# Optimization experiments

Measured on AMD Instinct MI355X. Metric: run time of the kernel, lower is better.

## Reference

```python
import jax, jax.numpy as jnp
import numpy as np

C = 32
C_Z = 128
S = 256   # MSA depth
N = 384   # residues


def setup_inputs() -> dict:
    key = jax.random.key(0)
    ks = jax.random.split(key, 7)
    m = jax.random.normal(ks[0], (S, N, C), dtype=jnp.float32)
    gamma = jnp.ones((C,), dtype=jnp.float32)
    beta = jnp.zeros((C,), dtype=jnp.float32)
    # projections stored as [in, out]
    W1 = jax.random.normal(ks[1], (C, C), dtype=jnp.float32) / np.sqrt(C)
    W2 = jax.random.normal(ks[2], (C, C), dtype=jnp.float32) / np.sqrt(C)
    W3 = jax.random.normal(ks[3], (C * C, C_Z), dtype=jnp.float32) / np.sqrt(C * C)
    b3 = jnp.zeros((C_Z,), dtype=jnp.float32)
    return {"m": m, "gamma": gamma, "beta": beta, "W1": W1, "W2": W2, "W3": W3, "b3": b3}


def reference(m, gamma, beta, W1, W2, W3, b3):
    # LayerNorm over channel dim
    mu = jnp.mean(m, axis=-1, keepdims=True)
    var = jnp.mean(jnp.square(m - mu), axis=-1, keepdims=True)
    mn = (m - mu) * jax.lax.rsqrt(var + 1e-5) * gamma + beta
    a = jnp.einsum('sic,cd->sid', mn, W1)  # [s, n, c]
    b = jnp.einsum('sic,cd->sid', mn, W2)  # [s, n, c]
    # outer product, mean over MSA dim s -> [n, n, c, c]
    o = jnp.einsum('sic,sjd->ijcd', a, b) / a.shape[0]
    o = o.reshape(o.shape[0], o.shape[1], C * C)  # [n, n, c*c]
    z = o @ W3 + b3  # [n, n, c_z]
    return z
```

## Files before the change

kernel.cpp:

```cpp
#include <hip/hip_runtime.h>

#define S_DEPTH 256
#define NRES 384
#define CIN 32
#define CZ 128
#define MDIM (NRES * CIN)

typedef short bf16x8 __attribute__((ext_vector_type(8)));
typedef short short4v __attribute__((ext_vector_type(4)));
typedef float f32x4 __attribute__((ext_vector_type(4)));

static __device__ __forceinline__ unsigned short f2bf(float f) {
  unsigned int u = __float_as_uint(f);
  unsigned int r = (u + 0x7fffu + ((u >> 16) & 1u)) >> 16;
  return (unsigned short)r;
}

static __device__ __forceinline__ void gld16(const void* g, void* l) {
  __builtin_amdgcn_global_load_lds((__attribute__((address_space(1))) void*)(g),
                                   (__attribute__((address_space(3))) void*)(l),
                                   16, 0, 0);
}

__global__ __launch_bounds__(256) void k_pre(
    const float* __restrict__ mm, const float* __restrict__ gamma,
    const float* __restrict__ beta, const float* __restrict__ W1,
    const float* __restrict__ W2, const float* __restrict__ W3,
    unsigned short* __restrict__ aT, unsigned short* __restrict__ bT,
    unsigned short* __restrict__ W3T) {
  __shared__ __align__(16) char sraw[256 * 33 * 4];
  const int t = threadIdx.x;

  if (blockIdx.x < 16) {
    unsigned short (*tile)[72] = (unsigned short(*)[72])sraw;
    const int b = blockIdx.x;
    const int d0 = (b & 7) * 4;
    const int e0 = (b >> 3) * 64;
#pragma unroll
    for (int iter = 0; iter < 32; ++iter) {
      int lr_ = iter * 4 + (t >> 6);
      int c = lr_ >> 2, dl = lr_ & 3;
      int q = c * 32 + d0 + dl;
      tile[lr_][t & 63] = f2bf(W3[q * 128 + e0 + (t & 63)]);
    }
    __syncthreads();
    const int e_l = t >> 2;
    const int dl = t & 3;
    unsigned short* dst = W3T + (((size_t)(d0 + dl) * 128) + e0 + e_l) * 32;
#pragma unroll
    for (int j = 0; j < 32; ++j) dst[j] = tile[j * 4 + dl][e_l];
    return;
  }

  float* buf = (float*)sraw;
  const int i = blockIdx.x - 16;

#pragma unroll
  for (int it = 0; it < 8; ++it) {
    int s = it * 32 + (t >> 3);
    int c4 = (t & 7) * 4;
    const float4 v = *(const float4*)(mm + ((size_t)s * NRES + i) * CIN + c4);
    buf[s * 33 + c4 + 0] = v.x;
    buf[s * 33 + c4 + 1] = v.y;
    buf[s * 33 + c4 + 2] = v.z;
    buf[s * 33 + c4 + 3] = v.w;
  }
  __syncthreads();

  float x[32];
#pragma unroll
  for (int k = 0; k < 32; ++k) x[k] = buf[t * 33 + k];
  float mu = 0.f;
#pragma unroll
  for (int k = 0; k < 32; ++k) mu += x[k];
  mu *= (1.f / 32.f);
  float var = 0.f;
#pragma unroll
  for (int k = 0; k < 32; ++k) {
    float dk = x[k] - mu;
    var += dk * dk;
  }
  var *= (1.f / 32.f);
  float inv = rsqrtf(var + 1e-5f);
#pragma unroll
  for (int k = 0; k < 32; ++k) x[k] = (x[k] - mu) * inv * gamma[k] + beta[k];

  float va[32], vb[32];
#pragma unroll
  for (int c = 0; c < 32; ++c) { va[c] = 0.f; vb[c] = 0.f; }
#pragma unroll
  for (int k = 0; k < 32; ++k) {
    float xk = x[k];
#pragma unroll
    for (int c = 0; c < 32; ++c) va[c] += xk * W1[k * 32 + c];
#pragma unroll
    for (int c = 0; c < 32; ++c) vb[c] += xk * W2[k * 32 + c];
  }

  unsigned short* dstA = aT + ((size_t)(t >> 6) * MDIM + (size_t)i * 32) * 64 + (t & 63);
  unsigned short* dstB = bT + ((size_t)(t >> 6) * MDIM + (size_t)i * 32) * 64 + (t & 63);
#pragma unroll
  for (int c = 0; c < 32; ++c) dstA[c * 64] = f2bf(va[c]);
#pragma unroll
  for (int c = 0; c < 32; ++c) dstB[c * 64] = f2bf(vb[c]);
}

__global__ __launch_bounds__(512, 2) void k_opm(
    const unsigned short* __restrict__ aT, const unsigned short* __restrict__ bT,
    const unsigned short* __restrict__ W3T, const float* __restrict__ b3,
    float* __restrict__ out) {
  __shared__ __align__(16) char smem[131072];
  const int t = threadIdx.x;
  const int w = t >> 6;
  const int l = t & 63;
  const int lr = l & 15;
  const int quad = l >> 4;
  const int wm = w >> 2, wn = w & 3;

  const int g = blockIdx.x;
  const int xcd = g & 7;
  const int rr = g >> 3;
  const int bx = rr / 6;
  const int by = xcd * 6 + (rr - bx * 6);
  const int m0 = by * 256;
  const int n0 = bx * 256;

  f32x4 acc[8][4];
#pragma unroll
  for (int mt = 0; mt < 8; ++mt)
#pragma unroll
    for (int nt = 0; nt < 4; ++nt) {
      acc[mt][nt][0] = 0.f; acc[mt][nt][1] = 0.f;
      acc[mt][nt][2] = 0.f; acc[mt][nt][3] = 0.f;
    }

  char* smemB = smem + 32768;
  const int laneoff = (l >> 3) * 64 + (((l & 7) ^ (l >> 3)) * 8);
  const int r8 = lr & 7;

  for (int k0 = 0; k0 < 256; k0 += 64) {
    __syncthreads();
    const unsigned short* aSlab = aT + ((size_t)(k0 >> 6) * MDIM + m0) * 64;
    const unsigned short* bSlab = bT + ((size_t)(k0 >> 6) * MDIM + n0) * 64;
#pragma unroll
    for (int p_ = 0; p_ < 4; ++p_) {
      int ch = p_ * 8 + w;
      gld16(aSlab + ch * 512 + laneoff, smem + ch * 1024);
    }
#pragma unroll
    for (int p_ = 0; p_ < 4; ++p_) {
      int ch = p_ * 8 + w;
      gld16(bSlab + ch * 512 + laneoff, smemB + ch * 1024);
    }
    __syncthreads();

#pragma unroll
    for (int ks = 0; ks < 2; ++ks) {
      const int segoff = (((ks * 4 + quad) ^ r8) << 4);
      bf16x8 af[8];
#pragma unroll
      for (int mt = 0; mt < 8; ++mt) {
        int chunk = wm * 16 + mt * 2 + (lr >> 3);
        af[mt] = *(const bf16x8*)(smem + chunk * 1024 + r8 * 128 + segoff);
      }
#pragma unroll
      for (int nt = 0; nt < 4; ++nt) {
        int chunk = wn * 8 + nt * 2 + (lr >> 3);
        bf16x8 bfr = *(const bf16x8*)(smemB + chunk * 1024 + r8 * 128 + segoff);
#pragma unroll
        for (int mt = 0; mt < 8; ++mt)
          acc[mt][nt] =
              __builtin_amdgcn_mfma_f32_16x16x32_bf16(af[mt], bfr, acc[mt][nt], 0, 0, 0);
      }
    }
  }

  __syncthreads();
  const float scale = 1.0f / 256.0f;
#pragma unroll
  for (int mt = 0; mt < 8; ++mt) {
    int i_l = wm * 4 + (mt >> 1);
    int chc = 2 * (mt & 1) + (quad >> 1);
#pragma unroll
    for (int nt = 0; nt < 4; ++nt) {
      int j_l = wn * 2 + (nt >> 1);
      int d = (nt & 1) * 16 + lr;
      int p = i_l * 8 + j_l;
      int ch = d * 4 + chc;
      int key = (p ^ d) & 7;
      int off = p * 2048 + ((ch ^ key) << 4) + 8 * (quad & 1);
      short4v pk;
      pk[0] = (short)f2bf(acc[mt][nt][0] * scale);
      pk[1] = (short)f2bf(acc[mt][nt][1] * scale);
      pk[2] = (short)f2bf(acc[mt][nt][2] * scale);
      pk[3] = (short)f2bf(acc[mt][nt][3] * scale);
      *(short4v*)(smem + off) = pk;
    }
  }
  __syncthreads();

  f32x4 zacc[4];
#pragma unroll
  for (int a = 0; a < 4; ++a) {
    zacc[a][0] = 0.f; zacc[a][1] = 0.f; zacc[a][2] = 0.f; zacc[a][3] = 0.f;
  }
  const float bias = b3[w * 16 + lr];

  const unsigned short* wg = W3T + (size_t)(w * 16 + lr) * 32 + quad * 8;

  bf16x8 wcur = *(const bf16x8*)(wg);
#pragma unroll
  for (int kq = 0; kq < 32; ++kq) {
    bf16x8 wnxt;
    if (kq < 31) wnxt = *(const bf16x8*)(wg + (size_t)(kq + 1) * 4096);
    bf16x8 aef[4];
#pragma unroll
    for (int mte = 0; mte < 4; ++mte) {
      int row = mte * 16 + lr;
      int ch = kq * 4 + quad;
      int key = (row ^ kq) & 7;
      aef[mte] = *(const bf16x8*)(smem + row * 2048 + ((ch ^ key) << 4));
    }
#pragma unroll
    for (int mte = 0; mte < 4; ++mte)
      zacc[mte] = __builtin_amdgcn_mfma_f32_16x16x32_bf16(aef[mte], wcur, zacc[mte], 0, 0, 0);
    wcur = wnxt;
  }

  const int i0 = by * 8, j0 = bx * 8;
  const int e = w * 16 + lr;
#pragma unroll
  for (int mte = 0; mte < 4; ++mte)
#pragma unroll
    for (int r = 0; r < 4; ++r) {
      int p = mte * 16 + quad * 4 + r;
      out[(((size_t)(i0 + (p >> 3))) * NRES + (j0 + (p & 7))) * CZ + e] =
          zacc[mte][r] + bias;
    }
}

extern "C" void kernel_launch(void* const* d_in, const int* in_sizes, int n_in,
                              void* d_out, int out_size, void* d_ws, size_t ws_size,
                              hipStream_t stream) {
  const float* m = (const float*)d_in[0];
  const float* gamma = (const float*)d_in[1];
  const float* beta = (const float*)d_in[2];
  const float* W1 = (const float*)d_in[3];
  const float* W2 = (const float*)d_in[4];
  const float* W3 = (const float*)d_in[5];
  const float* b3 = (const float*)d_in[6];
  float* out = (float*)d_out;

  unsigned short* aT = (unsigned short*)d_ws;
  unsigned short* bT = aT + (size_t)MDIM * S_DEPTH;
  unsigned short* W3T = bT + (size_t)MDIM * S_DEPTH;

  k_pre<<<400, 256, 0, stream>>>(m, gamma, beta, W1, W2, W3, aT, bT, W3T);
  k_opm<<<2304, 512, 0, stream>>>(aT, bT, W3T, b3, out);
}
```

Measured before the change: 237.9 us.

## Double-buffer OPM K-loop, split preprocessing blocks, retile W3 projection

The main outer-product GEMM loop now double-buffers the A/B slabs in LDS, so the next K-slab loads while MFMAs run on the current one, with one barrier per iteration. The preprocessing kernel is split 4x per residue, one block per MSA-depth quarter with each thread handling 8 output channels, raising its block count to improve parallelism. The W3 projection stage is retiled so each wave computes a 2x2 MFMA tile instead of 4x1, reusing each LDS A fragment across two W3 columns. The cost is that LDS use in the GEMM phase doubles to the full 128KB, and the preprocessing now recomputes LayerNorm per channel group.

```diff
diff --git a/kernel.cpp b/kernel.cpp
--- a/kernel.cpp
+++ b/kernel.cpp
@@ -28,7 +28,7 @@
     const float* __restrict__ W2, const float* __restrict__ W3,
     unsigned short* __restrict__ aT, unsigned short* __restrict__ bT,
     unsigned short* __restrict__ W3T) {
-  __shared__ __align__(16) char sraw[256 * 33 * 4];
+  __shared__ __align__(16) char sraw[128 * 72 * 2];
   const int t = threadIdx.x;
 
   if (blockIdx.x < 16) {
@@ -53,23 +53,27 @@
   }
 
   float* buf = (float*)sraw;
-  const int i = blockIdx.x - 16;
-
-#pragma unroll
-  for (int it = 0; it < 8; ++it) {
-    int s = it * 32 + (t >> 3);
-    int c4 = (t & 7) * 4;
-    const float4 v = *(const float4*)(mm + ((size_t)s * NRES + i) * CIN + c4);
-    buf[s * 33 + c4 + 0] = v.x;
-    buf[s * 33 + c4 + 1] = v.y;
-    buf[s * 33 + c4 + 2] = v.z;
-    buf[s * 33 + c4 + 3] = v.w;
+  const int b = blockIdx.x - 16;
+  const int i = b >> 2;
+  const int g = b & 3;
+
+  {
+    int r = t >> 2, c8 = (t & 3) * 8;
+    const float* src = mm + ((size_t)(g * 64 + r) * NRES + i) * CIN + c8;
+    const float4 v0 = *(const float4*)(src);
+    const float4 v1 = *(const float4*)(src + 4);
+    float* d = buf + r * 33 + c8;
+    d[0] = v0.x; d[1] = v0.y; d[2] = v0.z; d[3] = v0.w;
+    d[4] = v1.x; d[5] = v1.y; d[6] = v1.z; d[7] = v1.w;
   }
   __syncthreads();
 
+  const int row = t & 63;
+  const int cg = t >> 6;
+
   float x[32];
 #pragma unroll
-  for (int k = 0; k < 32; ++k) x[k] = buf[t * 33 + k];
+  for (int k = 0; k < 32; ++k) x[k] = buf[row * 33 + k];
   float mu = 0.f;
 #pragma unroll
   for (int k = 0; k < 32; ++k) mu += x[k];
@@ -85,24 +89,28 @@
 #pragma unroll
   for (int k = 0; k < 32; ++k) x[k] = (x[k] - mu) * inv * gamma[k] + beta[k];
 
-  float va[32], vb[32];
-#pragma unroll
-  for (int c = 0; c < 32; ++c) { va[c] = 0.f; vb[c] = 0.f; }
+  float va[8], vb[8];
+#pragma unroll
+  for (int c = 0; c < 8; ++c) { va[c] = 0.f; vb[c] = 0.f; }
 #pragma unroll
   for (int k = 0; k < 32; ++k) {
     float xk = x[k];
-#pragma unroll
-    for (int c = 0; c < 32; ++c) va[c] += xk * W1[k * 32 + c];
-#pragma unroll
-    for (int c = 0; c < 32; ++c) vb[c] += xk * W2[k * 32 + c];
-  }
-
-  unsigned short* dstA = aT + ((size_t)(t >> 6) * MDIM + (size_t)i * 32) * 64 + (t & 63);
-  unsigned short* dstB = bT + ((size_t)(t >> 6) * MDIM + (size_t)i * 32) * 64 + (t & 63);
-#pragma unroll
-  for (int c = 0; c < 32; ++c) dstA[c * 64] = f2bf(va[c]);
-#pragma unroll
-  for (int c = 0; c < 32; ++c) dstB[c * 64] = f2bf(vb[c]);
+    const float* w1r = W1 + k * 32 + cg * 8;
+    const float* w2r = W2 + k * 32 + cg * 8;
+#pragma unroll
+    for (int c = 0; c < 8; ++c) va[c] += xk * w1r[c];
+#pragma unroll
+    for (int c = 0; c < 8; ++c) vb[c] += xk * w2r[c];
+  }
+
+  unsigned short* dstA =
+      aT + ((size_t)g * MDIM + (size_t)i * 32 + cg * 8) * 64 + row;
+  unsigned short* dstB =
+      bT + ((size_t)g * MDIM + (size_t)i * 32 + cg * 8) * 64 + row;
+#pragma unroll
+  for (int c = 0; c < 8; ++c) dstA[c * 64] = f2bf(va[c]);
+#pragma unroll
+  for (int c = 0; c < 8; ++c) dstB[c * 64] = f2bf(vb[c]);
 }
 
 __global__ __launch_bounds__(512, 2) void k_opm(
@@ -134,25 +142,35 @@
       acc[mt][nt][2] = 0.f; acc[mt][nt][3] = 0.f;
     }
 
-  char* smemB = smem + 32768;
   const int laneoff = (l >> 3) * 64 + (((l & 7) ^ (l >> 3)) * 8);
   const int r8 = lr & 7;
 
-  for (int k0 = 0; k0 < 256; k0 += 64) {
-    __syncthreads();
-    const unsigned short* aSlab = aT + ((size_t)(k0 >> 6) * MDIM + m0) * 64;
-    const unsigned short* bSlab = bT + ((size_t)(k0 >> 6) * MDIM + n0) * 64;
+  {
+    const unsigned short* aS = aT + (size_t)m0 * 64;
+    const unsigned short* bS = bT + (size_t)n0 * 64;
 #pragma unroll
     for (int p_ = 0; p_ < 4; ++p_) {
       int ch = p_ * 8 + w;
-      gld16(aSlab + ch * 512 + laneoff, smem + ch * 1024);
-    }
-#pragma unroll
-    for (int p_ = 0; p_ < 4; ++p_) {
-      int ch = p_ * 8 + w;
-      gld16(bSlab + ch * 512 + laneoff, smemB + ch * 1024);
-    }
-    __syncthreads();
+      gld16(aS + ch * 512 + laneoff, smem + ch * 1024);
+      gld16(bS + ch * 512 + laneoff, smem + 32768 + ch * 1024);
+    }
+  }
+  __syncthreads();
+
+  for (int kt = 0; kt < 4; ++kt) {
+    if (kt < 3) {
+      char* nb = smem + ((kt + 1) & 1) * 65536;
+      const unsigned short* aS = aT + ((size_t)(kt + 1) * MDIM + m0) * 64;
+      const unsigned short* bS = bT + ((size_t)(kt + 1) * MDIM + n0) * 64;
+#pragma unroll
+      for (int p_ = 0; p_ < 4; ++p_) {
+        int ch = p_ * 8 + w;
+        gld16(aS + ch * 512 + laneoff, nb + ch * 1024);
+        gld16(bS + ch * 512 + laneoff, nb + 32768 + ch * 1024);
+      }
+    }
+    const char* cb = smem + (kt & 1) * 65536;
+    const char* cbB = cb + 32768;
 
 #pragma unroll
     for (int ks = 0; ks < 2; ++ks) {
@@ -161,21 +179,21 @@
 #pragma unroll
       for (int mt = 0; mt < 8; ++mt) {
         int chunk = wm * 16 + mt * 2 + (lr >> 3);
-        af[mt] = *(const bf16x8*)(smem + chunk * 1024 + r8 * 128 + segoff);
+        af[mt] = *(const bf16x8*)(cb + chunk * 1024 + r8 * 128 + segoff);
       }
 #pragma unroll
       for (int nt = 0; nt < 4; ++nt) {
         int chunk = wn * 8 + nt * 2 + (lr >> 3);
-        bf16x8 bfr = *(const bf16x8*)(smemB + chunk * 1024 + r8 * 128 + segoff);
+        bf16x8 bfr = *(const bf16x8*)(cbB + chunk * 1024 + r8 * 128 + segoff);
 #pragma unroll
         for (int mt = 0; mt < 8; ++mt)
           acc[mt][nt] =
               __builtin_amdgcn_mfma_f32_16x16x32_bf16(af[mt], bfr, acc[mt][nt], 0, 0, 0);
       }
     }
-  }
-
-  __syncthreads();
+    __syncthreads();
+  }
+
   const float scale = 1.0f / 256.0f;
 #pragma unroll
   for (int mt = 0; mt < 8; ++mt) {
@@ -199,43 +217,58 @@
   }
   __syncthreads();
 
-  f32x4 zacc[4];
-#pragma unroll
-  for (int a = 0; a < 4; ++a) {
-    zacc[a][0] = 0.f; zacc[a][1] = 0.f; zacc[a][2] = 0.f; zacc[a][3] = 0.f;
-  }
-  const float bias = b3[w * 16 + lr];
-
-  const unsigned short* wg = W3T + (size_t)(w * 16 + lr) * 32 + quad * 8;
-
-  bf16x8 wcur = *(const bf16x8*)(wg);
+  const int pb = w >> 2;
+  const int eb = w & 3;
+  f32x4 zacc[2][2];
+#pragma unroll
+  for (int a = 0; a < 2; ++a)
+#pragma unroll
+    for (int e_ = 0; e_ < 2; ++e_) {
+      zacc[a][e_][0] = 0.f; zacc[a][e_][1] = 0.f;
+      zacc[a][e_][2] = 0.f; zacc[a][e_][3] = 0.f;
+    }
+  const float bias0 = b3[eb * 32 + lr];
+  const float bias1 = b3[eb * 32 + 16 + lr];
+
+  const unsigned short* wg0 = W3T + (size_t)(eb * 32 + lr) * 32 + quad * 8;
+  const unsigned short* wg1 = wg0 + 512;
+
+  bf16x8 wc0 = *(const bf16x8*)(wg0);
+  bf16x8 wc1 = *(const bf16x8*)(wg1);
 #pragma unroll
   for (int kq = 0; kq < 32; ++kq) {
-    bf16x8 wnxt;
-    if (kq < 31) wnxt = *(const bf16x8*)(wg + (size_t)(kq + 1) * 4096);
-    bf16x8 aef[4];
-#pragma unroll
-    for (int mte = 0; mte < 4; ++mte) {
-      int row = mte * 16 + lr;
+    bf16x8 wn0, wn1;
+    if (kq < 31) {
+      wn0 = *(const bf16x8*)(wg0 + (size_t)(kq + 1) * 4096);
+      wn1 = *(const bf16x8*)(wg1 + (size_t)(kq + 1) * 4096);
+    }
+    bf16x8 aef[2];
+#pragma unroll
+    for (int mte = 0; mte < 2; ++mte) {
+      int row_ = pb * 32 + mte * 16 + lr;
       int ch = kq * 4 + quad;
-      int key = (row ^ kq) & 7;
-      aef[mte] = *(const bf16x8*)(smem + row * 2048 + ((ch ^ key) << 4));
-    }
-#pragma unroll
-    for (int mte = 0; mte < 4; ++mte)
-      zacc[mte] = __builtin_amdgcn_mfma_f32_16x16x32_bf16(aef[mte], wcur, zacc[mte], 0, 0, 0);
-    wcur = wnxt;
+      int key = (row_ ^ kq) & 7;
+      aef[mte] = *(const bf16x8*)(smem + row_ * 2048 + ((ch ^ key) << 4));
+    }
+#pragma unroll
+    for (int mte = 0; mte < 2; ++mte) {
+      zacc[mte][0] =
+          __builtin_amdgcn_mfma_f32_16x16x32_bf16(aef[mte], wc0, zacc[mte][0], 0, 0, 0);
+      zacc[mte][1] =
+          __builtin_amdgcn_mfma_f32_16x16x32_bf16(aef[mte], wc1, zacc[mte][1], 0, 0, 0);
+    }
+    wc0 = wn0; wc1 = wn1;
   }
 
   const int i0 = by * 8, j0 = bx * 8;
-  const int e = w * 16 + lr;
-#pragma unroll
-  for (int mte = 0; mte < 4; ++mte)
+#pragma unroll
+  for (int mte = 0; mte < 2; ++mte)
 #pragma unroll
     for (int r = 0; r < 4; ++r) {
-      int p = mte * 16 + quad * 4 + r;
-      out[(((size_t)(i0 + (p >> 3))) * NRES + (j0 + (p & 7))) * CZ + e] =
-          zacc[mte][r] + bias;
+      int p = pb * 32 + mte * 16 + quad * 4 + r;
+      size_t base = (((size_t)(i0 + (p >> 3))) * NRES + (j0 + (p & 7))) * CZ;
+      out[base + eb * 32 + lr] = zacc[mte][0][r] + bias0;
+      out[base + eb * 32 + 16 + lr] = zacc[mte][1][r] + bias1;
     }
 }
 
@@ -255,6 +288,6 @@
   unsigned short* bT = aT + (size_t)MDIM * S_DEPTH;
   unsigned short* W3T = bT + (size_t)MDIM * S_DEPTH;
 
-  k_pre<<<400, 256, 0, stream>>>(m, gamma, beta, W1, W2, W3, aT, bT, W3T);
+  k_pre<<<1552, 256, 0, stream>>>(m, gamma, beta, W1, W2, W3, aT, bT, W3T);
   k_opm<<<2304, 512, 0, stream>>>(aT, bT, W3T, b3, out);
 }
```

New measurement: 257.3 us. 1.08x slower.
